# Optimization experiments

Measured on AMD Instinct MI355X. Metric: run time of the kernel, lower is better.

The kernel has to match this reference:

```python
import jax, jax.numpy as jnp
import numpy as np

NUM_HEADS = 16
EPS = 1e-6
ROPE_THETA = 10000.0


def _rmsnorm_fp32(x, w):
    # RMSNorm computed in fp32, scale by learned weight (per head_dim)
    xf = x.astype(jnp.float32)
    var = jnp.mean(xf * xf, axis=-1, keepdims=True)
    return (xf * jax.lax.rsqrt(var + EPS) * w.astype(jnp.float32)).astype(x.dtype)


def _rope_3d_angles(T, H, W, head_dim):
    # split head_dim across (t,h,w) axes; all parts even
    dh = 2 * ((head_dim // 3) // 2)
    dw = dh
    dt = head_dim - dh - dw

    def axis_ang(L, d):
        inv = 1.0 / (ROPE_THETA ** (jnp.arange(0, d, 2, dtype=jnp.float32) / d))
        return jnp.arange(L, dtype=jnp.float32)[:, None] * inv[None, :]  # [L, d//2]

    at = axis_ang(T, dt)  # [T, dt/2]
    ah = axis_ang(H, dh)  # [H, dh/2]
    aw = axis_ang(W, dw)  # [W, dw/2]
    # broadcast to [T,H,W, head_dim//2] then flatten to [N, head_dim//2]
    at_g = jnp.broadcast_to(at[:, None, None, :], (T, H, W, dt // 2))
    ah_g = jnp.broadcast_to(ah[None, :, None, :], (T, H, W, dh // 2))
    aw_g = jnp.broadcast_to(aw[None, None, :, :], (T, H, W, dw // 2))
    ang = jnp.concatenate([at_g, ah_g, aw_g], axis=-1).reshape(T * H * W, head_dim // 2)
    return jnp.cos(ang), jnp.sin(ang)


def _apply_rope(x, cos, sin):
    # x: [B,Hh,N,D]; cos/sin: [N, D/2]; interleaved complex-pair rotation
    xr = x[..., 0::2]
    xi = x[..., 1::2]
    c = cos[None, None, :, :]
    s = sin[None, None, :, :]
    out_r = xr * c - xi * s
    out_i = xr * s + xi * c
    return jnp.stack([out_r, out_i], axis=-1).reshape(x.shape)


def setup_inputs() -> dict:
    key = jax.random.key(0)
    ks = jax.random.split(key, 7)
    dim, hd = 2048, 128
    x = jax.random.normal(ks[0], (1, 2048, dim), dtype=jnp.float32)
    qkv_w = jax.random.normal(ks[1], (3 * dim, dim), dtype=jnp.float32) * (dim ** -0.5)
    qkv_b = jax.random.normal(ks[2], (3 * dim,), dtype=jnp.float32) * 0.02
    proj_w = jax.random.normal(ks[3], (dim, dim), dtype=jnp.float32) * (dim ** -0.5)
    proj_b = jax.random.normal(ks[4], (dim,), dtype=jnp.float32) * 0.02
    q_norm_w = jnp.ones((hd,), dtype=jnp.float32)
    k_norm_w = jnp.ones((hd,), dtype=jnp.float32)
    return {"x": x, "qkv_w": qkv_w, "qkv_b": qkv_b, "proj_w": proj_w,
            "proj_b": proj_b, "q_norm_w": q_norm_w, "k_norm_w": k_norm_w,
            "t_dim": 8, "h_dim": 16, "w_dim": 16}


def reference(x, qkv_w, qkv_b, proj_w, proj_b, q_norm_w, k_norm_w, t_dim, h_dim, w_dim):
    B, N, C = x.shape
    Hh = NUM_HEADS
    D = C // Hh
    scale = D ** -0.5
    # QKV projection (torch Linear: x @ W.T + b)
    qkv = x @ qkv_w.T + qkv_b                      # [B,N,3C]
    qkv = qkv.reshape(B, N, 3, Hh, D).transpose(2, 0, 3, 1, 4)  # [3,B,Hh,N,D]
    q, k, v = qkv[0], qkv[1], qkv[2]
    q = _rmsnorm_fp32(q, q_norm_w)
    k = _rmsnorm_fp32(k, k_norm_w)
    cos, sin = _rope_3d_angles(t_dim, h_dim, w_dim, D)
    q = _apply_rope(q, cos, sin)
    k = _apply_rope(k, cos, sin)
    # SDPA (non-causal)
    scores = jnp.einsum('bhqd,bhkd->bhqk', q, k) * scale
    attn = jax.nn.softmax(scores, axis=-1)
    out = jnp.einsum('bhqk,bhkd->bhqd', attn, v)   # [B,Hh,N,D]
    out = out.transpose(0, 2, 1, 3).reshape(B, N, C)
    return out @ proj_w.T + proj_b
```

## Files before the change

### kernel.cpp

```cpp
#include <hip/hip_runtime.h>
#include <hip/hip_bf16.h>
#include <cstdint>
#include <cstddef>

typedef __attribute__((ext_vector_type(8))) short bf16x8;
typedef __attribute__((ext_vector_type(4))) float f32x4;
typedef __attribute__((ext_vector_type(16))) float f32x16;

#define AS1 __attribute__((address_space(1)))
#define AS3 __attribute__((address_space(3)))

__device__ __forceinline__ void gload_lds16(const void* g, void* l) {
  __builtin_amdgcn_global_load_lds((const AS1 void*)g, (AS3 void*)l, 16, 0, 0);
}

__device__ __forceinline__ unsigned short f2bf(float x) {
  __hip_bfloat16 h = __float2bfloat16(x);
  return __builtin_bit_cast(unsigned short, h);
}
__device__ __forceinline__ float bf2f(unsigned short u) {
  return __builtin_bit_cast(float, (unsigned int)u << 16);
}
__device__ __forceinline__ unsigned cvtpk(float a, float b) {
  unsigned r;
  asm("v_cvt_pk_bf16_f32 %0, %1, %2" : "=v"(r) : "v"(a), "v"(b));
  return r;
}
__device__ __forceinline__ void pswap(unsigned& x, unsigned& y) {
  asm volatile("v_permlane32_swap_b32 %0, %1" : "+v"(x), "+v"(y));
}

__global__ __launch_bounds__(256) void k_cvt3(const float* __restrict__ a, unsigned short* __restrict__ ao, int na4,
                                              const float* __restrict__ b, unsigned short* __restrict__ bo, int nb4,
                                              const float* __restrict__ c, unsigned short* __restrict__ co, int nc4) {
  const int stride = gridDim.x * 256;
  for (int i = blockIdx.x * 256 + threadIdx.x; i < na4; i += stride) {
    float4 v = reinterpret_cast<const float4*>(a)[i];
    ushort4 o; o.x = f2bf(v.x); o.y = f2bf(v.y); o.z = f2bf(v.z); o.w = f2bf(v.w);
    reinterpret_cast<ushort4*>(ao)[i] = o;
  }
  for (int i = blockIdx.x * 256 + threadIdx.x; i < nb4; i += stride) {
    float4 v = reinterpret_cast<const float4*>(b)[i];
    ushort4 o; o.x = f2bf(v.x); o.y = f2bf(v.y); o.z = f2bf(v.z); o.w = f2bf(v.w);
    reinterpret_cast<ushort4*>(bo)[i] = o;
  }
  for (int i = blockIdx.x * 256 + threadIdx.x; i < nc4; i += stride) {
    float4 v = reinterpret_cast<const float4*>(c)[i];
    ushort4 o; o.x = f2bf(v.x); o.y = f2bf(v.y); o.z = f2bf(v.z); o.w = f2bf(v.w);
    reinterpret_cast<ushort4*>(co)[i] = o;
  }
}

__global__ __launch_bounds__(256) void k_rope_tab(float* __restrict__ cosT,
                                                  float* __restrict__ sinT,
                                                  const int* __restrict__ hdim,
                                                  const int* __restrict__ wdim) {
  int idx = blockIdx.x * 256 + threadIdx.x;
  if (idx >= 2048 * 64) return;
  const int n = idx >> 6, j = idx & 63;
  const int H = *hdim, W = *wdim;
  const int w = n % W;
  const int rem = n / W;
  const int h = rem % H;
  const int t = rem / H;
  float pos, i2, d;
  if (j < 22)      { pos = (float)t; i2 = (float)(2 * j);        d = 44.f; }
  else if (j < 43) { pos = (float)h; i2 = (float)(2 * (j - 22)); d = 42.f; }
  else             { pos = (float)w; i2 = (float)(2 * (j - 43)); d = 42.f; }
  const float ang = pos * powf(10000.0f, -i2 / d);
  cosT[idx] = cosf(ang);
  sinT[idx] = sinf(ang);
}

__global__ __launch_bounds__(256, 2) void k_gemmQKV(const unsigned short* __restrict__ A,
                                                    const unsigned short* __restrict__ B,
                                                    const float* __restrict__ bias,
                                                    unsigned short* __restrict__ C,
                                                    int M, int N, int K) {
  __shared__ __align__(16) char lds[81920];
  const int tid = threadIdx.x;
  const int lane = tid & 63;
  const int wid = tid >> 6;
  const int wr = wid >> 1, wc = wid & 1;

  const int xcd = blockIdx.x & 7;
  const int t0 = blockIdx.x >> 3;
  const int bx = xcd * 4 + (t0 & 3);
  const int by = t0 >> 2;
  const int row0 = by * 128, col0 = bx * 192;
  const int NT = K >> 5;

  auto stageA = [&](int kcol0, char* slot) {
#pragma unroll
    for (int r = 0; r < 2; ++r) {
      const int off = r * 4096 + tid * 16;
      const int pair = off >> 7;
      const int un = (off & 127) ^ ((pair & 7) << 4);
      const int grow = pair * 2 + (un >> 6);
      gload_lds16(A + (size_t)(row0 + grow) * K + kcol0 + ((un & 63) >> 1),
                  slot + r * 4096 + wid * 1024);
    }
  };
  auto stageB = [&](int kcol0, char* slot) {
#pragma unroll
    for (int r = 0; r < 3; ++r) {
      const int off = r * 4096 + tid * 16;
      const int pair = off >> 7;
      const int un = (off & 127) ^ ((pair & 7) << 4);
      const int grow = pair * 2 + (un >> 6);
      gload_lds16(B + (size_t)(col0 + grow) * K + kcol0 + ((un & 63) >> 1),
                  slot + r * 4096 + wid * 1024);
    }
  };
  auto frag = [&](const char* slot, int r, int kb) -> bf16x8 {
    return *reinterpret_cast<const bf16x8*>(
        slot + (r >> 1) * 128 + ((((r & 1) << 6) + kb) ^ (((r >> 1) & 7) << 4)));
  };

  f32x4 acc[4][6];
#pragma unroll
  for (int i = 0; i < 4; ++i)
#pragma unroll
    for (int j = 0; j < 6; ++j) acc[i][j] = (f32x4){0.f, 0.f, 0.f, 0.f};

#pragma unroll
  for (int p = 0; p < 3; ++p) {
    stageA(p * 32, lds + p * 8192);
    stageB(p * 32, lds + 32768 + p * 12288);
  }
  asm volatile("s_waitcnt vmcnt(10)" ::: "memory");
  __builtin_amdgcn_s_barrier();

  const int kb = (lane >> 4) << 4;
  for (int j = 0; j < NT; ++j) {
    const char* baseA = lds + (j & 3) * 8192;
    const char* baseB = lds + 32768 + (j & 3) * 12288;
    bf16x8 af[4], bq[6];
#pragma unroll
    for (int fr = 0; fr < 4; ++fr) af[fr] = frag(baseA, wr * 64 + fr * 16 + (lane & 15), kb);
#pragma unroll
    for (int fc = 0; fc < 6; ++fc) bq[fc] = frag(baseB, wc * 96 + fc * 16 + (lane & 15), kb);

    const int jp = j + 3;
    if (jp < NT) {
      stageA(jp * 32, lds + (jp & 3) * 8192);
      stageB(jp * 32, lds + 32768 + (jp & 3) * 12288);
      asm volatile("s_waitcnt vmcnt(10)" ::: "memory");
    } else if (j + 2 < NT) {
      asm volatile("s_waitcnt vmcnt(5)" ::: "memory");
    } else if (j + 1 < NT) {
      asm volatile("s_waitcnt vmcnt(0)" ::: "memory");
    }
    if (j + 1 < NT) __builtin_amdgcn_s_barrier();

    __builtin_amdgcn_s_setprio(1);
#pragma unroll
    for (int fr = 0; fr < 4; ++fr)
#pragma unroll
      for (int fc = 0; fc < 6; ++fc)
        acc[fr][fc] = __builtin_amdgcn_mfma_f32_16x16x32_bf16(af[fr], bq[fc], acc[fr][fc], 0, 0, 0);
    __builtin_amdgcn_s_setprio(0);
  }

#pragma unroll
  for (int fr = 0; fr < 4; ++fr)
#pragma unroll
    for (int fc = 0; fc < 6; ++fc) {
      const int col = col0 + wc * 96 + fc * 16 + (lane & 15);
      const float bv = bias[col];
#pragma unroll
      for (int jj = 0; jj < 4; ++jj) {
        const int row = row0 + wr * 64 + fr * 16 + (lane >> 4) * 4 + jj;
        C[(size_t)row * N + col] = f2bf(acc[fr][fc][jj] + bv);
      }
    }
}

__global__ __launch_bounds__(256, 2) void k_gemmProj(const unsigned short* __restrict__ A,
                                                     const unsigned short* __restrict__ B,
                                                     float* __restrict__ Cp,
                                                     int M, int N, int K, int KS) {
  __shared__ __align__(16) char lds[65536];
  const int tid = threadIdx.x;
  const int lane = tid & 63;
  const int wid = tid >> 6;
  const int wr = wid >> 1, wc = wid & 1;
  const int row0 = blockIdx.y * 128;
  const int col0 = blockIdx.x * 128;
  const int k0 = blockIdx.z * KS;
  const int NT = KS >> 5;

  auto stageS = [&](const unsigned short* src, int grow0, int kcol0, char* slot) {
#pragma unroll
    for (int r = 0; r < 2; ++r) {
      const int off = r * 4096 + tid * 16;
      const int pair = off >> 7;
      const int un = (off & 127) ^ ((pair & 7) << 4);
      const int grow = pair * 2 + (un >> 6);
      gload_lds16(src + (size_t)(grow0 + grow) * K + kcol0 + ((un & 63) >> 1),
                  slot + r * 4096 + wid * 1024);
    }
  };
  auto frag = [&](const char* slot, int r, int kb) -> bf16x8 {
    return *reinterpret_cast<const bf16x8*>(
        slot + (r >> 1) * 128 + ((((r & 1) << 6) + kb) ^ (((r >> 1) & 7) << 4)));
  };

  f32x4 acc[4][4];
#pragma unroll
  for (int i = 0; i < 4; ++i)
#pragma unroll
    for (int j = 0; j < 4; ++j) acc[i][j] = (f32x4){0.f, 0.f, 0.f, 0.f};

#pragma unroll
  for (int p = 0; p < 3; ++p) {
    stageS(A, row0, k0 + p * 32, lds + p * 8192);
    stageS(B, col0, k0 + p * 32, lds + 32768 + p * 8192);
  }
  asm volatile("s_waitcnt vmcnt(8)" ::: "memory");
  __builtin_amdgcn_s_barrier();

  const int kb = (lane >> 4) << 4;
  for (int j = 0; j < NT; ++j) {
    const char* baseA = lds + (j & 3) * 8192;
    const char* baseB = lds + 32768 + (j & 3) * 8192;
    bf16x8 af[4], bq[4];
#pragma unroll
    for (int fr = 0; fr < 4; ++fr) af[fr] = frag(baseA, wr * 64 + fr * 16 + (lane & 15), kb);
#pragma unroll
    for (int fc = 0; fc < 4; ++fc) bq[fc] = frag(baseB, wc * 64 + fc * 16 + (lane & 15), kb);

    const int jp = j + 3;
    if (jp < NT) {
      stageS(A, row0, k0 + jp * 32, lds + (jp & 3) * 8192);
      stageS(B, col0, k0 + jp * 32, lds + 32768 + (jp & 3) * 8192);
      asm volatile("s_waitcnt vmcnt(8)" ::: "memory");
    } else if (j + 2 < NT) {
      asm volatile("s_waitcnt vmcnt(4)" ::: "memory");
    } else if (j + 1 < NT) {
      asm volatile("s_waitcnt vmcnt(0)" ::: "memory");
    }
    if (j + 1 < NT) __builtin_amdgcn_s_barrier();

    __builtin_amdgcn_s_setprio(1);
#pragma unroll
    for (int fr = 0; fr < 4; ++fr)
#pragma unroll
      for (int fc = 0; fc < 4; ++fc)
        acc[fr][fc] = __builtin_amdgcn_mfma_f32_16x16x32_bf16(af[fr], bq[fc], acc[fr][fc], 0, 0, 0);
    __builtin_amdgcn_s_setprio(0);
  }

  float* Cz = Cp + (size_t)blockIdx.z * M * N;
#pragma unroll
  for (int fr = 0; fr < 4; ++fr)
#pragma unroll
    for (int fc = 0; fc < 4; ++fc) {
      const int col = col0 + wc * 64 + fc * 16 + (lane & 15);
#pragma unroll
      for (int jj = 0; jj < 4; ++jj) {
        const int row = row0 + wr * 64 + fr * 16 + (lane >> 4) * 4 + jj;
        Cz[(size_t)row * N + col] = acc[fr][fc][jj];
      }
    }
}

__global__ __launch_bounds__(256) void k_addbias(const float* __restrict__ Cp,
                                                 const float* __restrict__ bias,
                                                 float* __restrict__ out) {
  const int i = blockIdx.x * 256 + threadIdx.x;
  const float4 a = reinterpret_cast<const float4*>(Cp)[i];
  const float4 b = reinterpret_cast<const float4*>(Cp + 2048ull * 2048)[i];
  const float4 bv = reinterpret_cast<const float4*>(bias)[i & 511];
  float4 o;
  o.x = a.x + b.x + bv.x; o.y = a.y + b.y + bv.y;
  o.z = a.z + b.z + bv.z; o.w = a.w + b.w + bv.w;
  reinterpret_cast<float4*>(out)[i] = o;
}

__global__ __launch_bounds__(256) void k_qk_post(const unsigned short* __restrict__ qkv,
                                                 const float* __restrict__ qw,
                                                 const float* __restrict__ kw,
                                                 const float* __restrict__ cosT,
                                                 const float* __restrict__ sinT,
                                                 unsigned short* __restrict__ qo,
                                                 unsigned short* __restrict__ ko) {
  const int lane = threadIdx.x & 63;
  const int wid = threadIdx.x >> 6;
  const int pair = blockIdx.x * 4 + wid;
  const int n = pair >> 4, h = pair & 15;
  const float c = cosT[n * 64 + lane];
  const float s = sinT[n * 64 + lane];
#pragma unroll
  for (int sq = 0; sq < 2; ++sq) {
    const unsigned short* src = qkv + (size_t)n * 6144 + sq * 2048 + h * 128;
    const unsigned int vp = reinterpret_cast<const unsigned int*>(src)[lane];
    const float vx = bf2f((unsigned short)(vp & 0xffff));
    const float vy = bf2f((unsigned short)(vp >> 16));
    float ss = vx * vx + vy * vy;
#pragma unroll
    for (int m = 1; m < 64; m <<= 1) ss += __shfl_xor(ss, m, 64);
    const float r = rsqrtf(ss * (1.0f / 128.0f) + 1e-6f);
    float2 wv = reinterpret_cast<const float2*>(sq == 0 ? qw : kw)[lane];
    const float xr = vx * r * wv.x;
    const float xi = vy * r * wv.y;
    float orr = xr * c - xi * s;
    float oi  = xr * s + xi * c;
    if (sq == 0) { orr *= 0.08838834764831845f; oi *= 0.08838834764831845f; }
    unsigned short* dst = (sq == 0 ? qo : ko) + ((size_t)h * 2048 + n) * 128 + 2 * lane;
    const unsigned int pk = (unsigned int)f2bf(orr) | ((unsigned int)f2bf(oi) << 16);
    *reinterpret_cast<unsigned int*>(dst) = pk;
  }
}

__global__ __launch_bounds__(256) void k_v_tr(const unsigned short* __restrict__ qkv,
                                              unsigned short* __restrict__ vt2) {
  __shared__ __align__(16) unsigned short tile[64][136];
  const int h = blockIdx.y;
  const int n0 = blockIdx.x * 64;
  const int t = threadIdx.x;
  {
    const int row = t >> 2;
    const int c0 = (t & 3) * 32;
    const unsigned short* src = qkv + (size_t)(n0 + row) * 6144 + 4096 + h * 128 + c0;
#pragma unroll
    for (int j = 0; j < 32; j += 8)
      *reinterpret_cast<bf16x8*>(&tile[row][c0 + j]) =
          *reinterpret_cast<const bf16x8*>(src + j);
  }
  __syncthreads();
#pragma unroll
  for (int g4 = 0; g4 < 4; ++g4) {
    const int g = g4 * 256 + t;
    const int c = g >> 8;
    const int dblk = (g >> 6) & 3;
    const int p = g & 63;
    const int d = dblk * 32 + (p & 31);
    const int hi = p >> 5;
    bf16x8 o;
#pragma unroll
    for (int e = 0; e < 8; ++e) o[e] = (short)tile[c * 16 + hi * 8 + e][d];
    const size_t oidx = ((((size_t)h * 128 + (n0 >> 4) + c) * 4 + dblk) * 64 + p) * 8;
    *reinterpret_cast<bf16x8*>(vt2 + oidx) = o;
  }
}

__global__ __launch_bounds__(256) void k_fattn(const unsigned short* __restrict__ q,
                                               const unsigned short* __restrict__ k,
                                               const unsigned short* __restrict__ vt2,
                                               unsigned short* __restrict__ Onorm,
                                               float* __restrict__ lseb) {
  __shared__ __align__(16) unsigned short Ks[2][64 * 128];
  __shared__ __align__(16) unsigned short Vs[2][64 * 128];
  const int lane = threadIdx.x & 63;
  const int wid = threadIdx.x >> 6;
  const int hi2 = lane >> 5;
  const int ql = lane & 31;
  const int bid = blockIdx.x;
  const int h = bid & 15;
  const int qb = (bid >> 4) & 15;
  const int ksp = bid >> 8;
  const int q0 = qb * 128 + wid * 32;
  const int kbase = ksp * 1024;

  auto stageK = [&](int buf, int kt2) {
#pragma unroll
    for (int r = 0; r < 4; ++r) {
      const int off = r * 4096 + (wid * 64 + lane) * 16;
      const int row = off >> 8;
      const int colb = (off & 255) ^ ((row & 15) << 4);
      gload_lds16(k + ((size_t)h * 2048 + kbase + kt2 * 64 + row) * 128 + (colb >> 1),
                  (char*)Ks[buf] + r * 4096 + wid * 1024);
    }
  };
  auto stageV = [&](int buf, int kt2) {
    const unsigned short* vbase = vt2 + ((size_t)h * 128 + (kbase >> 4) + kt2 * 4) * 2048;
#pragma unroll
    for (int r = 0; r < 4; ++r)
      gload_lds16(vbase + r * 2048 + (wid * 64 + lane) * 8,
                  (char*)Vs[buf] + r * 4096 + wid * 1024);
  };

  bf16x8 qf[8];
  {
    const unsigned short* qp = q + ((size_t)h * 2048 + q0 + ql) * 128 + hi2 * 8;
#pragma unroll
    for (int c = 0; c < 8; ++c) qf[c] = *reinterpret_cast<const bf16x8*>(qp + c * 16);
  }
  f32x16 O[4];
#pragma unroll
  for (int i = 0; i < 4; ++i)
#pragma unroll
    for (int j = 0; j < 16; ++j) O[i][j] = 0.f;
  float m = -1e30f, l = 0.f;

  stageK(0, 0);
  stageV(0, 0);
  asm volatile("s_waitcnt vmcnt(0)" ::: "memory");
  __builtin_amdgcn_s_barrier();

  const int kswz = (lane & 15) << 4;
  for (int kt = 0; kt < 16; ++kt) {
    const int cur = kt & 1;
    const bool pf = (kt + 1 < 16);
    if (pf) { stageK(cur ^ 1, kt + 1); stageV(cur ^ 1, kt + 1); }

    f32x16 s0, s1;
#pragma unroll
    for (int j = 0; j < 16; ++j) { s0[j] = 0.f; s1[j] = 0.f; }
    __builtin_amdgcn_s_setprio(1);
#pragma unroll
    for (int c = 0; c < 8; ++c) {
      bf16x8 a0 = *reinterpret_cast<const bf16x8*>(
          (const char*)Ks[cur] + ql * 256 + ((c * 32 + hi2 * 16) ^ kswz));
      s0 = __builtin_amdgcn_mfma_f32_32x32x16_bf16(a0, qf[c], s0, 0, 0, 0);
    }
#pragma unroll
    for (int c = 0; c < 8; ++c) {
      bf16x8 a1 = *reinterpret_cast<const bf16x8*>(
          (const char*)Ks[cur] + (32 + ql) * 256 + ((c * 32 + hi2 * 16) ^ kswz));
      s1 = __builtin_amdgcn_mfma_f32_32x32x16_bf16(a1, qf[c], s1, 0, 0, 0);
    }
    __builtin_amdgcn_s_setprio(0);

    float mt = s0[0];
#pragma unroll
    for (int j = 1; j < 16; ++j) mt = fmaxf(mt, s0[j]);
#pragma unroll
    for (int j = 0; j < 16; ++j) mt = fmaxf(mt, s1[j]);
    mt = fmaxf(mt, __shfl_xor(mt, 32, 64));

    if (!__all(mt <= m + 8.0f)) {
      const float mn = fmaxf(m, mt);
      const float al = __expf(m - mn);
      m = mn;
      l *= al;
#pragma unroll
      for (int i = 0; i < 4; ++i)
#pragma unroll
        for (int j = 0; j < 16; ++j) O[i][j] *= al;
    }
    float rs = 0.f;
#pragma unroll
    for (int j = 0; j < 16; ++j) {
      s0[j] = __expf(s0[j] - m); rs += s0[j];
      s1[j] = __expf(s1[j] - m); rs += s1[j];
    }
    rs += __shfl_xor(rs, 32, 64);
    l += rs;

    bf16x8 pfr[4];
#pragma unroll
    for (int half = 0; half < 2; ++half) {
      const f32x16& sv = half ? s1 : s0;
      unsigned a[8];
#pragma unroll
      for (int j2 = 0; j2 < 8; ++j2) a[j2] = cvtpk(sv[2 * j2], sv[2 * j2 + 1]);
      pswap(a[0], a[2]);
      pswap(a[1], a[3]);
      pswap(a[4], a[6]);
      pswap(a[5], a[7]);
      union { uint4 u; bf16x8 v; } p0, p1;
      p0.u.x = a[0]; p0.u.y = a[1]; p0.u.z = a[2]; p0.u.w = a[3];
      p1.u.x = a[4]; p1.u.y = a[5]; p1.u.z = a[6]; p1.u.w = a[7];
      pfr[half * 2 + 0] = p0.v;
      pfr[half * 2 + 1] = p1.v;
    }

    __builtin_amdgcn_s_setprio(1);
#pragma unroll
    for (int dblk = 0; dblk < 4; ++dblk) {
#pragma unroll
      for (int c2 = 0; c2 < 4; ++c2) {
        bf16x8 va = *reinterpret_cast<const bf16x8*>(
            (const char*)Vs[cur] + ((c2 * 4 + dblk) * 64 + lane) * 16);
        O[dblk] = __builtin_amdgcn_mfma_f32_32x32x16_bf16(va, pfr[c2], O[dblk], 0, 0, 0);
      }
    }
    __builtin_amdgcn_s_setprio(0);

    if (pf) {
      asm volatile("s_waitcnt vmcnt(0)" ::: "memory");
      __builtin_amdgcn_s_barrier();
    }
  }

  const float rl = 1.0f / l;
  const int n = q0 + ql;
  unsigned short* ob = Onorm + (((size_t)(ksp * 16 + h) * 2048) + n) * 128;
#pragma unroll
  for (int dblk = 0; dblk < 4; ++dblk)
#pragma unroll
    for (int a = 0; a < 4; ++a) {
      uint2 w;
      w.x = (unsigned)f2bf(O[dblk][a * 4 + 0] * rl) | ((unsigned)f2bf(O[dblk][a * 4 + 1] * rl) << 16);
      w.y = (unsigned)f2bf(O[dblk][a * 4 + 2] * rl) | ((unsigned)f2bf(O[dblk][a * 4 + 3] * rl) << 16);
      *reinterpret_cast<uint2*>(ob + dblk * 32 + a * 8 + hi2 * 4) = w;
    }
  if (hi2 == 0)
    lseb[(size_t)(ksp * 16 + h) * 2048 + n] = m + logf(l);
}

__global__ __launch_bounds__(256) void k_merge(const unsigned short* __restrict__ Onorm,
                                               const float* __restrict__ lseb,
                                               unsigned short* __restrict__ att) {
  const int idx = blockIdx.x * 256 + threadIdx.x;
  const int n = idx >> 8;
  const int r = idx & 255;
  const int h = r >> 4;
  const int d0 = (r & 15) * 8;
  const float l0 = lseb[(size_t)h * 2048 + n];
  const float l1 = lseb[(size_t)(16 + h) * 2048 + n];
  const float M = fmaxf(l0, l1);
  float w0 = __expf(l0 - M), w1 = __expf(l1 - M);
  const float inv = 1.0f / (w0 + w1);
  w0 *= inv; w1 *= inv;
  const bf16x8 o0 = *reinterpret_cast<const bf16x8*>(
      Onorm + ((size_t)h * 2048 + n) * 128 + d0);
  const bf16x8 o1 = *reinterpret_cast<const bf16x8*>(
      Onorm + ((size_t)(16 + h) * 2048 + n) * 128 + d0);
  bf16x8 o;
#pragma unroll
  for (int e = 0; e < 8; ++e)
    o[e] = (short)f2bf(bf2f((unsigned short)o0[e]) * w0 + bf2f((unsigned short)o1[e]) * w1);
  *reinterpret_cast<bf16x8*>(att + (size_t)n * 2048 + h * 128 + d0) = o;
}

extern "C" void kernel_launch(void* const* d_in, const int* in_sizes, int n_in,
                              void* d_out, int out_size, void* d_ws, size_t ws_size,
                              hipStream_t stream) {
  (void)in_sizes; (void)n_in; (void)out_size; (void)ws_size;
  const float* x      = (const float*)d_in[0];
  const float* qkv_w  = (const float*)d_in[1];
  const float* qkv_b  = (const float*)d_in[2];
  const float* proj_w = (const float*)d_in[3];
  const float* proj_b = (const float*)d_in[4];
  const float* q_nw   = (const float*)d_in[5];
  const float* k_nw   = (const float*)d_in[6];
  const int* h_dim    = (const int*)d_in[8];
  const int* w_dim    = (const int*)d_in[9];
  float* out = (float*)d_out;

  char* ws = (char*)d_ws;
  size_t off = 0;
  auto carve = [&](size_t bytes) -> void* {
    void* p = ws + off;
    off += (bytes + 255) & ~(size_t)255;
    return p;
  };
  unsigned short* x_bf   = (unsigned short*)carve(2048ull * 2048 * 2);
  unsigned short* w1_bf  = (unsigned short*)carve(6144ull * 2048 * 2);
  unsigned short* w2_bf  = (unsigned short*)carve(2048ull * 2048 * 2);
  unsigned short* qkvb   = (unsigned short*)carve(2048ull * 6144 * 2);
  unsigned short* q_bf   = (unsigned short*)carve(16ull * 2048 * 128 * 2);
  unsigned short* k_bf   = (unsigned short*)carve(16ull * 2048 * 128 * 2);
  unsigned short* vt2_bf = (unsigned short*)carve(16ull * 2048 * 128 * 2);
  unsigned short* att_bf = (unsigned short*)carve(2048ull * 2048 * 2);
  unsigned short* on_bf  = (unsigned short*)carve(2ull * 16 * 2048 * 128 * 2);
  float*          lseb   = (float*)carve(2ull * 16 * 2048 * 4);
  float*          projp  = (float*)carve(2ull * 2048 * 2048 * 4);
  float*          cosT   = (float*)carve(2048ull * 64 * 4);
  float*          sinT   = (float*)carve(2048ull * 64 * 4);

  hipLaunchKernelGGL(k_cvt3, dim3(2048), dim3(256), 0, stream,
                     x, x_bf, 2048 * 2048 / 4,
                     qkv_w, w1_bf, 6144 * 2048 / 4,
                     proj_w, w2_bf, 2048 * 2048 / 4);
  hipLaunchKernelGGL(k_rope_tab, dim3(512), dim3(256), 0, stream, cosT, sinT, h_dim, w_dim);
  hipLaunchKernelGGL(k_gemmQKV, dim3(512), dim3(256), 0, stream,
                     x_bf, w1_bf, qkv_b, qkvb, 2048, 6144, 2048);
  hipLaunchKernelGGL(k_qk_post, dim3(8192), dim3(256), 0, stream,
                     qkvb, q_nw, k_nw, cosT, sinT, q_bf, k_bf);
  hipLaunchKernelGGL(k_v_tr, dim3(32, 16), dim3(256), 0, stream, qkvb, vt2_bf);
  hipLaunchKernelGGL(k_fattn, dim3(512), dim3(256), 0, stream,
                     q_bf, k_bf, vt2_bf, on_bf, lseb);
  hipLaunchKernelGGL(k_merge, dim3(2048), dim3(256), 0, stream, on_bf, lseb, att_bf);
  hipLaunchKernelGGL(k_gemmProj, dim3(16, 16, 2), dim3(256), 0, stream,
                     att_bf, w2_bf, projp, 2048, 2048, 2048, 1024);
  hipLaunchKernelGGL(k_addbias, dim3(4096), dim3(256), 0, stream, projp, proj_b, out);
}
```

Before: 175.5 us.

## Fuse rope table, QK/V post, and remove proj split-K with fused bias

```diff
diff --git a/kernel.cpp b/kernel.cpp
--- a/kernel.cpp
+++ b/kernel.cpp
@@ -32,7 +32,9 @@
 
 __global__ __launch_bounds__(256) void k_cvt3(const float* __restrict__ a, unsigned short* __restrict__ ao, int na4,
                                               const float* __restrict__ b, unsigned short* __restrict__ bo, int nb4,
-                                              const float* __restrict__ c, unsigned short* __restrict__ co, int nc4) {
+                                              const float* __restrict__ c, unsigned short* __restrict__ co, int nc4,
+                                              float* __restrict__ cosT, float* __restrict__ sinT,
+                                              const int* __restrict__ hdim, const int* __restrict__ wdim) {
   const int stride = gridDim.x * 256;
   for (int i = blockIdx.x * 256 + threadIdx.x; i < na4; i += stride) {
     float4 v = reinterpret_cast<const float4*>(a)[i];
@@ -49,27 +51,21 @@
     ushort4 o; o.x = f2bf(v.x); o.y = f2bf(v.y); o.z = f2bf(v.z); o.w = f2bf(v.w);
     reinterpret_cast<ushort4*>(co)[i] = o;
   }
-}
-
-__global__ __launch_bounds__(256) void k_rope_tab(float* __restrict__ cosT,
-                                                  float* __restrict__ sinT,
-                                                  const int* __restrict__ hdim,
-                                                  const int* __restrict__ wdim) {
-  int idx = blockIdx.x * 256 + threadIdx.x;
-  if (idx >= 2048 * 64) return;
-  const int n = idx >> 6, j = idx & 63;
   const int H = *hdim, W = *wdim;
-  const int w = n % W;
-  const int rem = n / W;
-  const int h = rem % H;
-  const int t = rem / H;
-  float pos, i2, d;
-  if (j < 22)      { pos = (float)t; i2 = (float)(2 * j);        d = 44.f; }
-  else if (j < 43) { pos = (float)h; i2 = (float)(2 * (j - 22)); d = 42.f; }
-  else             { pos = (float)w; i2 = (float)(2 * (j - 43)); d = 42.f; }
-  const float ang = pos * powf(10000.0f, -i2 / d);
-  cosT[idx] = cosf(ang);
-  sinT[idx] = sinf(ang);
+  for (int idx = blockIdx.x * 256 + threadIdx.x; idx < 2048 * 64; idx += stride) {
+    const int n = idx >> 6, j = idx & 63;
+    const int w = n % W;
+    const int rem = n / W;
+    const int h = rem % H;
+    const int t = rem / H;
+    float pos, i2, d;
+    if (j < 22)      { pos = (float)t; i2 = (float)(2 * j);        d = 44.f; }
+    else if (j < 43) { pos = (float)h; i2 = (float)(2 * (j - 22)); d = 42.f; }
+    else             { pos = (float)w; i2 = (float)(2 * (j - 43)); d = 42.f; }
+    const float ang = pos * powf(10000.0f, -i2 / d);
+    cosT[idx] = cosf(ang);
+    sinT[idx] = sinf(ang);
+  }
 }
 
 __global__ __launch_bounds__(256, 2) void k_gemmQKV(const unsigned short* __restrict__ A,
@@ -178,26 +174,34 @@
 
 __global__ __launch_bounds__(256, 2) void k_gemmProj(const unsigned short* __restrict__ A,
                                                      const unsigned short* __restrict__ B,
-                                                     float* __restrict__ Cp,
-                                                     int M, int N, int K, int KS) {
-  __shared__ __align__(16) char lds[65536];
+                                                     const float* __restrict__ bias,
+                                                     float* __restrict__ out,
+                                                     int M, int N, int K) {
+  __shared__ __align__(16) char lds[49152];
   const int tid = threadIdx.x;
   const int lane = tid & 63;
   const int wid = tid >> 6;
   const int wr = wid >> 1, wc = wid & 1;
-  const int row0 = blockIdx.y * 128;
+  const int row0 = blockIdx.y * 64;
   const int col0 = blockIdx.x * 128;
-  const int k0 = blockIdx.z * KS;
-  const int NT = KS >> 5;
-
-  auto stageS = [&](const unsigned short* src, int grow0, int kcol0, char* slot) {
+  const int NT = K >> 5;
+
+  auto stageA = [&](int kcol0, char* slot) {
+    const int off = tid * 16;
+    const int pair = off >> 7;
+    const int un = (off & 127) ^ ((pair & 7) << 4);
+    const int grow = pair * 2 + (un >> 6);
+    gload_lds16(A + (size_t)(row0 + grow) * K + kcol0 + ((un & 63) >> 1),
+                slot + wid * 1024);
+  };
+  auto stageB = [&](int kcol0, char* slot) {
 #pragma unroll
     for (int r = 0; r < 2; ++r) {
       const int off = r * 4096 + tid * 16;
       const int pair = off >> 7;
       const int un = (off & 127) ^ ((pair & 7) << 4);
       const int grow = pair * 2 + (un >> 6);
-      gload_lds16(src + (size_t)(grow0 + grow) * K + kcol0 + ((un & 63) >> 1),
+      gload_lds16(B + (size_t)(col0 + grow) * K + kcol0 + ((un & 63) >> 1),
                   slot + r * 4096 + wid * 1024);
     }
   };
@@ -206,37 +210,37 @@
         slot + (r >> 1) * 128 + ((((r & 1) << 6) + kb) ^ (((r >> 1) & 7) << 4)));
   };
 
-  f32x4 acc[4][4];
-#pragma unroll
-  for (int i = 0; i < 4; ++i)
+  f32x4 acc[2][4];
+#pragma unroll
+  for (int i = 0; i < 2; ++i)
 #pragma unroll
     for (int j = 0; j < 4; ++j) acc[i][j] = (f32x4){0.f, 0.f, 0.f, 0.f};
 
 #pragma unroll
   for (int p = 0; p < 3; ++p) {
-    stageS(A, row0, k0 + p * 32, lds + p * 8192);
-    stageS(B, col0, k0 + p * 32, lds + 32768 + p * 8192);
-  }
-  asm volatile("s_waitcnt vmcnt(8)" ::: "memory");
+    stageA(p * 32, lds + p * 4096);
+    stageB(p * 32, lds + 16384 + p * 8192);
+  }
+  asm volatile("s_waitcnt vmcnt(6)" ::: "memory");
   __builtin_amdgcn_s_barrier();
 
   const int kb = (lane >> 4) << 4;
   for (int j = 0; j < NT; ++j) {
-    const char* baseA = lds + (j & 3) * 8192;
-    const char* baseB = lds + 32768 + (j & 3) * 8192;
-    bf16x8 af[4], bq[4];
-#pragma unroll
-    for (int fr = 0; fr < 4; ++fr) af[fr] = frag(baseA, wr * 64 + fr * 16 + (lane & 15), kb);
+    const char* baseA = lds + (j & 3) * 4096;
+    const char* baseB = lds + 16384 + (j & 3) * 8192;
+    bf16x8 af[2], bq[4];
+#pragma unroll
+    for (int fr = 0; fr < 2; ++fr) af[fr] = frag(baseA, wr * 32 + fr * 16 + (lane & 15), kb);
 #pragma unroll
     for (int fc = 0; fc < 4; ++fc) bq[fc] = frag(baseB, wc * 64 + fc * 16 + (lane & 15), kb);
 
     const int jp = j + 3;
     if (jp < NT) {
-      stageS(A, row0, k0 + jp * 32, lds + (jp & 3) * 8192);
-      stageS(B, col0, k0 + jp * 32, lds + 32768 + (jp & 3) * 8192);
-      asm volatile("s_waitcnt vmcnt(8)" ::: "memory");
+      stageA(jp * 32, lds + (jp & 3) * 4096);
+      stageB(jp * 32, lds + 16384 + (jp & 3) * 8192);
+      asm volatile("s_waitcnt vmcnt(6)" ::: "memory");
     } else if (j + 2 < NT) {
-      asm volatile("s_waitcnt vmcnt(4)" ::: "memory");
+      asm volatile("s_waitcnt vmcnt(3)" ::: "memory");
     } else if (j + 1 < NT) {
       asm volatile("s_waitcnt vmcnt(0)" ::: "memory");
     }
@@ -244,104 +248,92 @@
 
     __builtin_amdgcn_s_setprio(1);
 #pragma unroll
-    for (int fr = 0; fr < 4; ++fr)
+    for (int fr = 0; fr < 2; ++fr)
 #pragma unroll
       for (int fc = 0; fc < 4; ++fc)
         acc[fr][fc] = __builtin_amdgcn_mfma_f32_16x16x32_bf16(af[fr], bq[fc], acc[fr][fc], 0, 0, 0);
     __builtin_amdgcn_s_setprio(0);
   }
 
-  float* Cz = Cp + (size_t)blockIdx.z * M * N;
-#pragma unroll
-  for (int fr = 0; fr < 4; ++fr)
+#pragma unroll
+  for (int fr = 0; fr < 2; ++fr)
 #pragma unroll
     for (int fc = 0; fc < 4; ++fc) {
       const int col = col0 + wc * 64 + fc * 16 + (lane & 15);
+      const float bv = bias[col];
 #pragma unroll
       for (int jj = 0; jj < 4; ++jj) {
-        const int row = row0 + wr * 64 + fr * 16 + (lane >> 4) * 4 + jj;
-        Cz[(size_t)row * N + col] = acc[fr][fc][jj];
+        const int row = row0 + wr * 32 + fr * 16 + (lane >> 4) * 4 + jj;
+        out[(size_t)row * N + col] = acc[fr][fc][jj] + bv;
       }
     }
 }
 
-__global__ __launch_bounds__(256) void k_addbias(const float* __restrict__ Cp,
-                                                 const float* __restrict__ bias,
-                                                 float* __restrict__ out) {
-  const int i = blockIdx.x * 256 + threadIdx.x;
-  const float4 a = reinterpret_cast<const float4*>(Cp)[i];
-  const float4 b = reinterpret_cast<const float4*>(Cp + 2048ull * 2048)[i];
-  const float4 bv = reinterpret_cast<const float4*>(bias)[i & 511];
-  float4 o;
-  o.x = a.x + b.x + bv.x; o.y = a.y + b.y + bv.y;
-  o.z = a.z + b.z + bv.z; o.w = a.w + b.w + bv.w;
-  reinterpret_cast<float4*>(out)[i] = o;
-}
-
-__global__ __launch_bounds__(256) void k_qk_post(const unsigned short* __restrict__ qkv,
-                                                 const float* __restrict__ qw,
-                                                 const float* __restrict__ kw,
-                                                 const float* __restrict__ cosT,
-                                                 const float* __restrict__ sinT,
-                                                 unsigned short* __restrict__ qo,
-                                                 unsigned short* __restrict__ ko) {
-  const int lane = threadIdx.x & 63;
-  const int wid = threadIdx.x >> 6;
-  const int pair = blockIdx.x * 4 + wid;
-  const int n = pair >> 4, h = pair & 15;
-  const float c = cosT[n * 64 + lane];
-  const float s = sinT[n * 64 + lane];
-#pragma unroll
-  for (int sq = 0; sq < 2; ++sq) {
-    const unsigned short* src = qkv + (size_t)n * 6144 + sq * 2048 + h * 128;
-    const unsigned int vp = reinterpret_cast<const unsigned int*>(src)[lane];
-    const float vx = bf2f((unsigned short)(vp & 0xffff));
-    const float vy = bf2f((unsigned short)(vp >> 16));
-    float ss = vx * vx + vy * vy;
-#pragma unroll
-    for (int m = 1; m < 64; m <<= 1) ss += __shfl_xor(ss, m, 64);
-    const float r = rsqrtf(ss * (1.0f / 128.0f) + 1e-6f);
-    float2 wv = reinterpret_cast<const float2*>(sq == 0 ? qw : kw)[lane];
-    const float xr = vx * r * wv.x;
-    const float xi = vy * r * wv.y;
-    float orr = xr * c - xi * s;
-    float oi  = xr * s + xi * c;
-    if (sq == 0) { orr *= 0.08838834764831845f; oi *= 0.08838834764831845f; }
-    unsigned short* dst = (sq == 0 ? qo : ko) + ((size_t)h * 2048 + n) * 128 + 2 * lane;
-    const unsigned int pk = (unsigned int)f2bf(orr) | ((unsigned int)f2bf(oi) << 16);
-    *reinterpret_cast<unsigned int*>(dst) = pk;
-  }
-}
-
-__global__ __launch_bounds__(256) void k_v_tr(const unsigned short* __restrict__ qkv,
+__global__ __launch_bounds__(256) void k_post(const unsigned short* __restrict__ qkv,
+                                              const float* __restrict__ qw,
+                                              const float* __restrict__ kw,
+                                              const float* __restrict__ cosT,
+                                              const float* __restrict__ sinT,
+                                              unsigned short* __restrict__ qo,
+                                              unsigned short* __restrict__ ko,
                                               unsigned short* __restrict__ vt2) {
   __shared__ __align__(16) unsigned short tile[64][136];
-  const int h = blockIdx.y;
-  const int n0 = blockIdx.x * 64;
-  const int t = threadIdx.x;
-  {
-    const int row = t >> 2;
-    const int c0 = (t & 3) * 32;
-    const unsigned short* src = qkv + (size_t)(n0 + row) * 6144 + 4096 + h * 128 + c0;
-#pragma unroll
-    for (int j = 0; j < 32; j += 8)
-      *reinterpret_cast<bf16x8*>(&tile[row][c0 + j]) =
-          *reinterpret_cast<const bf16x8*>(src + j);
-  }
-  __syncthreads();
-#pragma unroll
-  for (int g4 = 0; g4 < 4; ++g4) {
-    const int g = g4 * 256 + t;
-    const int c = g >> 8;
-    const int dblk = (g >> 6) & 3;
-    const int p = g & 63;
-    const int d = dblk * 32 + (p & 31);
-    const int hi = p >> 5;
-    bf16x8 o;
-#pragma unroll
-    for (int e = 0; e < 8; ++e) o[e] = (short)tile[c * 16 + hi * 8 + e][d];
-    const size_t oidx = ((((size_t)h * 128 + (n0 >> 4) + c) * 4 + dblk) * 64 + p) * 8;
-    *reinterpret_cast<bf16x8*>(vt2 + oidx) = o;
+  if (blockIdx.x < 8192) {
+    const int lane = threadIdx.x & 63;
+    const int wid = threadIdx.x >> 6;
+    const int pair = blockIdx.x * 4 + wid;
+    const int n = pair >> 4, h = pair & 15;
+    const float c = cosT[n * 64 + lane];
+    const float s = sinT[n * 64 + lane];
+#pragma unroll
+    for (int sq = 0; sq < 2; ++sq) {
+      const unsigned short* src = qkv + (size_t)n * 6144 + sq * 2048 + h * 128;
+      const unsigned int vp = reinterpret_cast<const unsigned int*>(src)[lane];
+      const float vx = bf2f((unsigned short)(vp & 0xffff));
+      const float vy = bf2f((unsigned short)(vp >> 16));
+      float ss = vx * vx + vy * vy;
+#pragma unroll
+      for (int m = 1; m < 64; m <<= 1) ss += __shfl_xor(ss, m, 64);
+      const float r = rsqrtf(ss * (1.0f / 128.0f) + 1e-6f);
+      float2 wv = reinterpret_cast<const float2*>(sq == 0 ? qw : kw)[lane];
+      const float xr = vx * r * wv.x;
+      const float xi = vy * r * wv.y;
+      float orr = xr * c - xi * s;
+      float oi  = xr * s + xi * c;
+      if (sq == 0) { orr *= 0.08838834764831845f; oi *= 0.08838834764831845f; }
+      unsigned short* dst = (sq == 0 ? qo : ko) + ((size_t)h * 2048 + n) * 128 + 2 * lane;
+      const unsigned int pk = (unsigned int)f2bf(orr) | ((unsigned int)f2bf(oi) << 16);
+      *reinterpret_cast<unsigned int*>(dst) = pk;
+    }
+  } else {
+    const int idx = blockIdx.x - 8192;
+    const int h = idx >> 5;
+    const int n0 = (idx & 31) * 64;
+    const int t = threadIdx.x;
+    {
+      const int row = t >> 2;
+      const int c0 = (t & 3) * 32;
+      const unsigned short* src = qkv + (size_t)(n0 + row) * 6144 + 4096 + h * 128 + c0;
+#pragma unroll
+      for (int j = 0; j < 32; j += 8)
+        *reinterpret_cast<bf16x8*>(&tile[row][c0 + j]) =
+            *reinterpret_cast<const bf16x8*>(src + j);
+    }
+    __syncthreads();
+#pragma unroll
+    for (int g4 = 0; g4 < 4; ++g4) {
+      const int g = g4 * 256 + t;
+      const int c = g >> 8;
+      const int dblk = (g >> 6) & 3;
+      const int p = g & 63;
+      const int d = dblk * 32 + (p & 31);
+      const int hi = p >> 5;
+      bf16x8 o;
+#pragma unroll
+      for (int e = 0; e < 8; ++e) o[e] = (short)tile[c * 16 + hi * 8 + e][d];
+      const size_t oidx = ((((size_t)h * 128 + (n0 >> 4) + c) * 4 + dblk) * 64 + p) * 8;
+      *reinterpret_cast<bf16x8*>(vt2 + oidx) = o;
+    }
   }
 }
 
@@ -558,24 +550,21 @@
   unsigned short* att_bf = (unsigned short*)carve(2048ull * 2048 * 2);
   unsigned short* on_bf  = (unsigned short*)carve(2ull * 16 * 2048 * 128 * 2);
   float*          lseb   = (float*)carve(2ull * 16 * 2048 * 4);
-  float*          projp  = (float*)carve(2ull * 2048 * 2048 * 4);
   float*          cosT   = (float*)carve(2048ull * 64 * 4);
   float*          sinT   = (float*)carve(2048ull * 64 * 4);
 
   hipLaunchKernelGGL(k_cvt3, dim3(2048), dim3(256), 0, stream,
                      x, x_bf, 2048 * 2048 / 4,
                      qkv_w, w1_bf, 6144 * 2048 / 4,
-                     proj_w, w2_bf, 2048 * 2048 / 4);
-  hipLaunchKernelGGL(k_rope_tab, dim3(512), dim3(256), 0, stream, cosT, sinT, h_dim, w_dim);
+                     proj_w, w2_bf, 2048 * 2048 / 4,
+                     cosT, sinT, h_dim, w_dim);
   hipLaunchKernelGGL(k_gemmQKV, dim3(512), dim3(256), 0, stream,
                      x_bf, w1_bf, qkv_b, qkvb, 2048, 6144, 2048);
-  hipLaunchKernelGGL(k_qk_post, dim3(8192), dim3(256), 0, stream,
-                     qkvb, q_nw, k_nw, cosT, sinT, q_bf, k_bf);
-  hipLaunchKernelGGL(k_v_tr, dim3(32, 16), dim3(256), 0, stream, qkvb, vt2_bf);
+  hipLaunchKernelGGL(k_post, dim3(8704), dim3(256), 0, stream,
+                     qkvb, q_nw, k_nw, cosT, sinT, q_bf, k_bf, vt2_bf);
   hipLaunchKernelGGL(k_fattn, dim3(512), dim3(256), 0, stream,
                      q_bf, k_bf, vt2_bf, on_bf, lseb);
   hipLaunchKernelGGL(k_merge, dim3(2048), dim3(256), 0, stream, on_bf, lseb, att_bf);
-  hipLaunchKernelGGL(k_gemmProj, dim3(16, 16, 2), dim3(256), 0, stream,
-                     att_bf, w2_bf, projp, 2048, 2048, 2048, 1024);
-  hipLaunchKernelGGL(k_addbias, dim3(4096), dim3(256), 0, stream, projp, proj_b, out);
-}
+  hipLaunchKernelGGL(k_gemmProj, dim3(16, 32), dim3(256), 0, stream,
+                     att_bf, w2_bf, proj_b, out, 2048, 2048, 2048);
+}
```

Result: faster. 166.4 us (median of 2 runs) (-5.2%).
